# Kernel optimization log

Measured on AMD Instinct MI355X. Metric: run time of the kernel, lower is better.

## Reference

```python
import jax, jax.numpy as jnp
import numpy as np

N, E, F_IN = 100000, 3200000, 512
H1, D1, C = 8, 8, 16  # layer1 heads, per-head dim; layer2 out classes
NEG_SLOPE = 0.2


def _segment_softmax(e, dst, num_segments):
    # numerically-stable softmax over edges grouped by destination node
    m = jax.ops.segment_max(e, dst, num_segments=num_segments)
    ex = jnp.exp(e - m[dst])
    s = jax.ops.segment_sum(ex, dst, num_segments=num_segments)
    return ex / (s[dst] + 1e-16)


def _gat_layer(x, src, dst, W, a_src, a_dst, heads, d_out):
    n = x.shape[0]
    h = (x @ W).reshape(n, heads, d_out)          # [N,H,D]
    al_s = jnp.einsum('nhd,hd->nh', h, a_src)     # [N,H]
    al_d = jnp.einsum('nhd,hd->nh', h, a_dst)
    e = jax.nn.leaky_relu(al_s[src] + al_d[dst], NEG_SLOPE)  # [E,H]
    alpha = _segment_softmax(e, dst, n)           # [E,H]
    msg = h[src] * alpha[..., None]               # [E,H,D]
    return jax.ops.segment_sum(msg, dst, num_segments=n)  # [N,H,D]


def setup_inputs() -> dict:
    key = jax.random.key(0)
    ks = jax.random.split(key, 8)
    x = jax.random.normal(ks[0], (N, F_IN), dtype=jnp.float32)
    edge_index = jax.random.randint(ks[1], (2, E), 0, N, dtype=jnp.int64)
    W1 = jax.random.normal(ks[2], (F_IN, H1 * D1), dtype=jnp.float32) * (1.0 / np.sqrt(F_IN))
    a1_src = jax.random.normal(ks[3], (H1, D1), dtype=jnp.float32)
    a1_dst = jax.random.normal(ks[4], (H1, D1), dtype=jnp.float32)
    W2 = jax.random.normal(ks[5], (H1 * D1, C), dtype=jnp.float32) * (1.0 / np.sqrt(H1 * D1))
    a2_src = jax.random.normal(ks[6], (1, C), dtype=jnp.float32)
    a2_dst = jax.random.normal(ks[7], (1, C), dtype=jnp.float32)
    return {'x': x, 'edge_index': edge_index, 'W1': W1, 'a1_src': a1_src,
            'a1_dst': a1_dst, 'W2': W2, 'a2_src': a2_src, 'a2_dst': a2_dst}


def reference(x, edge_index, W1, a1_src, a1_dst, W2, a2_src, a2_dst):
    src, dst = edge_index[0], edge_index[1]
    # layer 1: 8 heads, concat, then ELU (dropout is identity in eval mode)
    h1 = _gat_layer(x, src, dst, W1, a1_src, a1_dst, H1, D1)  # [N,H1,D1]
    h1 = jax.nn.elu(h1.reshape(N, H1 * D1))                   # [N,64]
    # layer 2: single head -> class logits
    h2 = _gat_layer(h1, src, dst, W2, a2_src, a2_dst, 1, C)   # [N,1,C]
    return jax.nn.log_softmax(h2.reshape(N, C), axis=1)
```

## Files before the change

### kernel.cpp

```cpp
#include <hip/hip_runtime.h>
#include <math.h>

#define NEG 0.2f
#define NB 64
#define BCAP 128

typedef __attribute__((ext_vector_type(8))) short bf16x8;
typedef __attribute__((ext_vector_type(4))) float f32x4;
typedef unsigned long long ull;

static __device__ __forceinline__ float lrelu(float x){ return x > 0.f ? x : NEG*x; }

static __device__ __forceinline__ void bsplit(float v, unsigned int& hi, unsigned int& lo){
  unsigned int u = __float_as_uint(v);
  unsigned int hb = (u + 0x7fffu + ((u >> 16) & 1u)) & 0xffff0000u;
  float hf = __uint_as_float(hb);
  float l = v - hf;
  unsigned int ul = __float_as_uint(l);
  hi = hb >> 16;
  lo = (ul + 0x7fffu + ((ul >> 16) & 1u)) >> 16;
}

static __device__ __forceinline__ float bf2f(unsigned short u){
  return __uint_as_float(((unsigned int)u) << 16);
}
static __device__ __forceinline__ unsigned short f2bf(float v){
  unsigned int u = __float_as_uint(v);
  return (unsigned short)((u + 0x7fffu + ((u >> 16) & 1u)) >> 16);
}

static __device__ __forceinline__ void split8(float4 v0, float4 v1, bf16x8& h, bf16x8& l){
  float vv[8] = {v0.x, v0.y, v0.z, v0.w, v1.x, v1.y, v1.z, v1.w};
  #pragma unroll
  for (int i = 0; i < 8; ++i) {
    unsigned int hi, lo;
    bsplit(vv[i], hi, lo);
    h[i] = (short)hi;
    l[i] = (short)lo;
  }
}

__global__ void k_zero(int* __restrict__ p, int n){
  int i = blockIdx.x*blockDim.x + threadIdx.x;
  if (i < n) p[i] = 0;
}

__global__ void k_flag(const int* __restrict__ u, int* __restrict__ flag){
  if (threadIdx.x == 0 && blockIdx.x == 0) {
    int z = 1;
    for (int e = 0; e < 64; ++e) if (u[2*e+1] != 0) { z = 0; break; }
    *flag = z;
  }
}

__global__ __launch_bounds__(256) void k_part(const int* __restrict__ u,
    const int* __restrict__ flag, int* __restrict__ pcur,
    ull* __restrict__ part, int E, int n, int SEGCAP){
  __shared__ ull buf[NB][BCAP];
  __shared__ int bcnt[NB];
  __shared__ int binc[NB];
  __shared__ int bbase;
  __shared__ int nflush;
  __shared__ unsigned char flist[NB];
  const bool f = (*flag) != 0;
  const int tid = threadIdx.x;
  const int g = blockIdx.x & 7;
  if (tid < NB) bcnt[tid] = 0;
  const long long stride = (long long)gridDim.x * 256;
  const long long iters = ((long long)E + stride - 1) / stride;
  long long e = (long long)blockIdx.x*256 + tid;
  for (long long it = 0; it < iters; ++it, e += stride) {
    if (tid < NB) binc[tid] = 0;
    if (tid == 0) nflush = 0;
    __syncthreads();
    int src = 0, dst = 0, b = 0;
    const bool valid = (e < E);
    if (valid) {
      src = f ? u[2*e] : u[e];
      dst = f ? u[2*(E+e)] : u[E+e];
      b = (int)(((long long)dst * NB) / n);
      atomicAdd(&binc[b], 1);
    }
    __syncthreads();
    if (tid < NB && bcnt[tid] > 0 && bcnt[tid] + binc[tid] > BCAP) {
      int i = atomicAdd(&nflush, 1);
      flist[i] = (unsigned char)tid;
    }
    __syncthreads();
    for (int i = 0; i < nflush; ++i) {
      int b2 = flist[i];
      int c = bcnt[b2]; if (c > BCAP) c = BCAP;
      if (tid == 0) bbase = atomicAdd(&pcur[(b2*8+g)*16], c);
      __syncthreads();
      int base = bbase;
      for (int j = tid; j < c; j += 256) {
        int pos = base + j;
        if (pos < SEGCAP) part[(size_t)(b2*8+g)*SEGCAP + pos] = buf[b2][j];
      }
      __syncthreads();
      if (tid == 0) bcnt[b2] = 0;
      __syncthreads();
    }
    if (valid) {
      int pos = atomicAdd(&bcnt[b], 1);
      if (pos < BCAP) buf[b][pos] = (ull)(unsigned)src | ((ull)(unsigned)dst << 32);
    }
    __syncthreads();
  }
  for (int b2 = 0; b2 < NB; ++b2) {
    int c = bcnt[b2]; if (c > BCAP) c = BCAP;
    if (c > 0) {
      if (tid == 0) bbase = atomicAdd(&pcur[(b2*8+g)*16], c);
      __syncthreads();
      int base = bbase;
      for (int j = tid; j < c; j += 256) {
        int pos = base + j;
        if (pos < SEGCAP) part[(size_t)(b2*8+g)*SEGCAP + pos] = buf[b2][j];
      }
    }
    __syncthreads();
  }
}

__global__ __launch_bounds__(1024) void k_histL(const int* __restrict__ pcur,
    const ull* __restrict__ part, int* __restrict__ cnt, int n, int SEGCAP){
  __shared__ int lcnt[1664];
  const int b = blockIdx.x;
  const int lo = (int)(((long long)b * n + NB - 1) / NB);
  const int hi = (int)(((long long)(b+1) * n + NB - 1) / NB);
  const int m = hi - lo;
  for (int i = threadIdx.x; i < m; i += 1024) lcnt[i] = 0;
  __syncthreads();
  for (int g = 0; g < 8; ++g) {
    int s = b*8 + g;
    int c = pcur[s*16]; if (c > SEGCAP) c = SEGCAP;
    for (int i = threadIdx.x; i < c; i += 1024) {
      ull v = __builtin_nontemporal_load(&part[(size_t)s*SEGCAP + i]);
      atomicAdd(&lcnt[(int)(unsigned)(v >> 32) - lo], 1);
    }
  }
  __syncthreads();
  for (int i = threadIdx.x; i < m; i += 1024) cnt[lo + i] = lcnt[i];
}

__global__ __launch_bounds__(256) void k_scan1(const int* __restrict__ cnt,
    int* __restrict__ ro, int* __restrict__ bsum, int n){
  int t = threadIdx.x;
  int base = blockIdx.x*1024 + t*4;
  int v0 = (base+0 < n) ? cnt[base+0] : 0;
  int v1 = (base+1 < n) ? cnt[base+1] : 0;
  int v2 = (base+2 < n) ? cnt[base+2] : 0;
  int v3 = (base+3 < n) ? cnt[base+3] : 0;
  int s = v0+v1+v2+v3;
  int lane = t & 63, w = t >> 6;
  int inc = s;
  for (int off = 1; off < 64; off <<= 1) {
    int tm = __shfl_up(inc, off);
    if (lane >= off) inc += tm;
  }
  __shared__ int wsum[4];
  if (lane == 63) wsum[w] = inc;
  __syncthreads();
  int wpre = 0;
  for (int k = 0; k < 4; ++k) if (k < w) wpre += wsum[k];
  int run = wpre + inc - s;
  if (base+0 < n) ro[base+0] = run; run += v0;
  if (base+1 < n) ro[base+1] = run; run += v1;
  if (base+2 < n) ro[base+2] = run; run += v2;
  if (base+3 < n) ro[base+3] = run; run += v3;
  if (t == 255) bsum[blockIdx.x] = run;
}

__global__ void k_scan2(int* __restrict__ bsum, int nb){
  int lane = threadIdx.x;
  int carry = 0;
  for (int b = 0; b < nb; b += 64) {
    int i = b + lane;
    int v = (i < nb) ? bsum[i] : 0;
    int inc = v;
    for (int off = 1; off < 64; off <<= 1) {
      int t = __shfl_up(inc, off);
      if (lane >= off) inc += t;
    }
    if (i < nb) bsum[i] = carry + inc - v;
    carry += __shfl(inc, 63);
  }
}

__global__ void k_scan3(int* __restrict__ ro, const int* __restrict__ bsum,
                        int n, int E){
  int i = blockIdx.x*blockDim.x + threadIdx.x;
  if (i < n) ro[i] = ro[i] + bsum[i >> 10];
  if (i == 0) ro[n] = E;
}

__global__ __launch_bounds__(1024) void k_fillL(const int* __restrict__ pcur,
    const ull* __restrict__ part, const int* __restrict__ ro,
    int* __restrict__ csr, int n, int SEGCAP){
  __shared__ int lcur[1664];
  const int b = blockIdx.x;
  const int lo = (int)(((long long)b * n + NB - 1) / NB);
  const int hi = (int)(((long long)(b+1) * n + NB - 1) / NB);
  const int m = hi - lo;
  for (int i = threadIdx.x; i < m; i += 1024) lcur[i] = ro[lo + i];
  __syncthreads();
  for (int g = 0; g < 8; ++g) {
    int s = b*8 + g;
    int c = pcur[s*16]; if (c > SEGCAP) c = SEGCAP;
    for (int i = threadIdx.x; i < c; i += 1024) {
      ull v = __builtin_nontemporal_load(&part[(size_t)s*SEGCAP + i]);
      int src = (int)(unsigned)v;
      int dst = (int)(unsigned)(v >> 32);
      int p = atomicAdd(&lcur[dst - lo], 1);
      csr[p] = src;
    }
  }
}

__global__ void k_wprep(const float* __restrict__ W1, unsigned short* __restrict__ wtH,
                        unsigned short* __restrict__ wtL){
  int i = blockIdx.x*256 + threadIdx.x;
  if (i >= 512*64) return;
  int k = i >> 6, c = i & 63;
  unsigned int hi, lo;
  bsplit(W1[i], hi, lo);
  wtH[c*512 + k] = (unsigned short)hi;
  wtL[c*512 + k] = (unsigned short)lo;
}

__global__ __launch_bounds__(256, 3) void k_proj1(const float* __restrict__ x,
    const unsigned short* __restrict__ wtH, const unsigned short* __restrict__ wtL,
    const float* __restrict__ a1s_g, const float* __restrict__ a1d_g,
    unsigned short* __restrict__ h1bf, float* __restrict__ al1s, float* __restrict__ al1d, int n){
  const int tid = threadIdx.x;
  const int lane = tid & 63;
  const int w = tid >> 6;
  const int l16 = lane & 15;
  const int lhi = lane >> 4;
  const int r0 = blockIdx.x*128 + w*32;

  float as_c[4], ad_c[4];
  #pragma unroll
  for (int f = 0; f < 4; ++f) { as_c[f] = a1s_g[16*f + l16]; ad_c[f] = a1d_g[16*f + l16]; }

  f32x4 acc[2][4];
  #pragma unroll
  for (int m = 0; m < 2; ++m)
    #pragma unroll
    for (int f = 0; f < 4; ++f) acc[m][f] = (f32x4){0.f,0.f,0.f,0.f};

  int rowA = r0 + l16;        if (rowA >= n) rowA = n - 1;
  int rowB = r0 + 16 + l16;   if (rowB >= n) rowB = n - 1;
  const float* xA = x + (size_t)rowA*512 + 8*lhi;
  const float* xB = x + (size_t)rowB*512 + 8*lhi;
  const unsigned short* wHp = wtH + (size_t)l16*512 + 8*lhi;
  const unsigned short* wLp = wtL + (size_t)l16*512 + 8*lhi;

  for (int k0 = 0; k0 < 512; k0 += 32) {
    float4 a0 = *(const float4*)(xA + k0);
    float4 a1v = *(const float4*)(xA + k0 + 4);
    float4 b0 = *(const float4*)(xB + k0);
    float4 b1v = *(const float4*)(xB + k0 + 4);
    bf16x8 bh[4], bl[4];
    #pragma unroll
    for (int f = 0; f < 4; ++f) {
      bh[f] = *(const bf16x8*)(wHp + (size_t)f*16*512 + k0);
      bl[f] = *(const bf16x8*)(wLp + (size_t)f*16*512 + k0);
    }
    bf16x8 ahA, alA, ahB, alB;
    split8(a0, a1v, ahA, alA);
    split8(b0, b1v, ahB, alB);
    #pragma unroll
    for (int f = 0; f < 4; ++f) {
      acc[0][f] = __builtin_amdgcn_mfma_f32_16x16x32_bf16(ahA, bh[f], acc[0][f], 0, 0, 0);
      acc[0][f] = __builtin_amdgcn_mfma_f32_16x16x32_bf16(ahA, bl[f], acc[0][f], 0, 0, 0);
      acc[0][f] = __builtin_amdgcn_mfma_f32_16x16x32_bf16(alA, bh[f], acc[0][f], 0, 0, 0);
      acc[1][f] = __builtin_amdgcn_mfma_f32_16x16x32_bf16(ahB, bh[f], acc[1][f], 0, 0, 0);
      acc[1][f] = __builtin_amdgcn_mfma_f32_16x16x32_bf16(ahB, bl[f], acc[1][f], 0, 0, 0);
      acc[1][f] = __builtin_amdgcn_mfma_f32_16x16x32_bf16(alB, bh[f], acc[1][f], 0, 0, 0);
    }
  }

  #pragma unroll
  for (int m = 0; m < 2; ++m) {
    #pragma unroll
    for (int r = 0; r < 4; ++r) {
      int node = r0 + 16*m + 4*lhi + r;
      bool ok = (node < n);
      #pragma unroll
      for (int f = 0; f < 4; ++f) {
        float v = acc[m][f][r];
        if (ok) h1bf[(size_t)node*64 + 16*f + l16] = f2bf(v);
        float vs = v * as_c[f], vd = v * ad_c[f];
        vs += __shfl_xor(vs, 1); vs += __shfl_xor(vs, 2); vs += __shfl_xor(vs, 4);
        vd += __shfl_xor(vd, 1); vd += __shfl_xor(vd, 2); vd += __shfl_xor(vd, 4);
        if (ok && (l16 & 7) == 0) {
          int head = 2*f + (l16 >> 3);
          al1s[node*8 + head] = vs;
          al1d[node*8 + head] = vd;
        }
      }
    }
  }
}

__global__ __launch_bounds__(256) void k_agg1(const int* __restrict__ ro,
    const int* __restrict__ csr, const float* __restrict__ al1s,
    const float* __restrict__ al1d, const unsigned short* __restrict__ h1bf,
    float* __restrict__ h1b, int n){
  int wid = blockIdx.x*4 + (threadIdx.x >> 6);
  if (wid >= n) return;
  int node = __builtin_amdgcn_readfirstlane(wid);
  int lane = threadIdx.x & 63;
  int h = lane >> 3;
  int beg = ro[node], end = ro[node+1];
  float ald = al1d[node*8 + h];
  float s = 0.f, acc = 0.f;
  if (beg < end) {
    int   srcb[4];
    float alb[4], hvb[4];
    #pragma unroll
    for (int j = 0; j < 4; ++j) {
      int idx = beg + j;
      srcb[j] = csr[idx < end ? idx : beg];
    }
    #pragma unroll
    for (int j = 0; j < 4; ++j) {
      alb[j] = al1s[srcb[j]*8 + h];
      hvb[j] = bf2f(h1bf[(size_t)srcb[j]*64 + lane]);
    }
    for (int t = beg; t < end; t += 4) {
      int   nsrc[4];
      float nal[4], nhv[4];
      #pragma unroll
      for (int j = 0; j < 4; ++j) {
        int idx = t + 4 + j;
        nsrc[j] = csr[idx < end ? idx : beg];
      }
      #pragma unroll
      for (int j = 0; j < 4; ++j) {
        nal[j] = al1s[nsrc[j]*8 + h];
        nhv[j] = bf2f(h1bf[(size_t)nsrc[j]*64 + lane]);
      }
      #pragma unroll
      for (int j = 0; j < 4; ++j) {
        float e = alb[j] + ald;
        e = e > 0.f ? e : NEG*e;
        float ex = (t + j < end) ? __expf(e) : 0.f;
        s += ex;
        acc = fmaf(hvb[j], ex, acc);
      }
      #pragma unroll
      for (int j = 0; j < 4; ++j) { srcb[j] = nsrc[j]; alb[j] = nal[j]; hvb[j] = nhv[j]; }
    }
  }
  float v = acc / (s + 1e-16f);
  v = v > 0.f ? v : expm1f(v);
  h1b[(size_t)node*64 + lane] = v;
}

__global__ __launch_bounds__(256) void k_proj2(const float* __restrict__ h1b,
    const float* __restrict__ W2, const float* __restrict__ a2s_g, const float* __restrict__ a2d_g,
    unsigned short* __restrict__ h2bf, float* __restrict__ al2s, float* __restrict__ al2d, int n){
  __shared__ float w[64*16];
  __shared__ float a2sv[16], a2dv[16];
  for (int i = threadIdx.x; i < 1024; i += 256) w[i] = W2[i];
  if (threadIdx.x < 16) { a2sv[threadIdx.x] = a2s_g[threadIdx.x]; a2dv[threadIdx.x] = a2d_g[threadIdx.x]; }
  __syncthreads();
  int c = threadIdx.x & 15;
  int nid = blockIdx.x*16 + (threadIdx.x >> 4);
  if (nid >= n) return;
  const float* row = h1b + (size_t)nid*64;
  float acc = 0.f;
  #pragma unroll
  for (int k0 = 0; k0 < 64; k0 += 4) {
    float4 r = *(const float4*)(row + k0);
    acc = fmaf(r.x, w[(k0+0)*16 + c], acc);
    acc = fmaf(r.y, w[(k0+1)*16 + c], acc);
    acc = fmaf(r.z, w[(k0+2)*16 + c], acc);
    acc = fmaf(r.w, w[(k0+3)*16 + c], acc);
  }
  h2bf[(size_t)nid*16 + c] = f2bf(acc);
  float vs = acc * a2sv[c], vd = acc * a2dv[c];
  vs += __shfl_xor(vs, 1); vs += __shfl_xor(vs, 2); vs += __shfl_xor(vs, 4); vs += __shfl_xor(vs, 8);
  vd += __shfl_xor(vd, 1); vd += __shfl_xor(vd, 2); vd += __shfl_xor(vd, 4); vd += __shfl_xor(vd, 8);
  if (c == 0) { al2s[nid] = vs; al2d[nid] = vd; }
}

__global__ __launch_bounds__(256) void k_agg2(const int* __restrict__ ro,
    const int* __restrict__ csr, const float* __restrict__ al2s,
    const float* __restrict__ al2d, const unsigned short* __restrict__ h2bf,
    float* __restrict__ out, int n){
  int wid = blockIdx.x*4 + (threadIdx.x >> 6);
  if (wid >= n) return;
  int node = __builtin_amdgcn_readfirstlane(wid);
  int lane = threadIdx.x & 63;
  int j = lane >> 4, c = lane & 15;
  int beg = ro[node], end = ro[node+1];
  float ald = al2d[node];
  float sp = 0.f, acc = 0.f;
  if (beg < end) {
    int i = beg + j;
    int sA = csr[i < end ? i : beg];
    float aA = al2s[sA];
    float hA = bf2f(h2bf[(size_t)sA*16 + c]);
    for (; i < end; i += 4) {
      int i2 = i + 4;
      int sB = csr[i2 < end ? i2 : beg];
      float aB = al2s[sB];
      float hB = bf2f(h2bf[(size_t)sB*16 + c]);
      float e = lrelu(aA + ald);
      float ex = __expf(e);
      sp += ex;
      acc = fmaf(ex, hA, acc);
      sA = sB; aA = aB; hA = hB;
    }
  }
  sp  += __shfl_xor(sp, 16);  sp  += __shfl_xor(sp, 32);
  acc += __shfl_xor(acc, 16); acc += __shfl_xor(acc, 32);
  float v = acc / (sp + 1e-16f);
  float mx = v;
  mx = fmaxf(mx, __shfl_xor(mx, 1)); mx = fmaxf(mx, __shfl_xor(mx, 2));
  mx = fmaxf(mx, __shfl_xor(mx, 4)); mx = fmaxf(mx, __shfl_xor(mx, 8));
  float l = v - mx;
  float se = __expf(l);
  se += __shfl_xor(se, 1); se += __shfl_xor(se, 2);
  se += __shfl_xor(se, 4); se += __shfl_xor(se, 8);
  float res = l - logf(se);
  if (j == 0) out[(size_t)node*16 + c] = res;
}

static inline size_t alignup(size_t x){ return (x + 255) & ~(size_t)255; }

extern "C" void kernel_launch(void* const* d_in, const int* in_sizes, int n_in,
                              void* d_out, int out_size, void* d_ws, size_t ws_size,
                              hipStream_t stream){
  const float* x   = (const float*)d_in[0];
  const int*   ei  = (const int*)  d_in[1];
  const float* W1  = (const float*)d_in[2];
  const float* a1s = (const float*)d_in[3];
  const float* a1d = (const float*)d_in[4];
  const float* W2  = (const float*)d_in[5];
  const float* a2s = (const float*)d_in[6];
  const float* a2d = (const float*)d_in[7];
  float* out = (float*)d_out;

  const int n = in_sizes[0] / 512;
  const int E = in_sizes[1] / 2;

  char* w = (char*)d_ws;
  unsigned short* h1bf = (unsigned short*)w; w += alignup((size_t)n*64*2);
  float* h1b  = (float*)w; w += alignup((size_t)n*64*4);
  float* al1s_ = (float*)w; w += alignup((size_t)n*8*4);
  float* al1d_ = (float*)w; w += alignup((size_t)n*8*4);
  unsigned short* h2bf = (unsigned short*)w; w += alignup((size_t)n*16*2);
  float* al2s_ = (float*)w; w += alignup((size_t)n*4);
  float* al2d_ = (float*)w; w += alignup((size_t)n*4);
  int* cnt    = (int*)w;   w += alignup((size_t)n*4);
  int* ro     = (int*)w;   w += alignup((size_t)(n+1)*4);
  int* csr    = (int*)w;   w += alignup((size_t)E*4);
  int* bsum   = (int*)w;   w += alignup(512*4);
  int* flag   = (int*)w;   w += alignup(64);
  int* pcur   = (int*)w;   w += alignup((size_t)NB*8*16*4);
  unsigned short* wtH = (unsigned short*)w; w += alignup(512*64*2);
  unsigned short* wtL = (unsigned short*)w; w += alignup(512*64*2);

  ull* part = (ull*)h1bf;
  const int SEGCAP = 9300;

  const int nb_scan = (n + 1023) / 1024;

  k_zero<<<(NB*8*16 + 255)/256, 256, 0, stream>>>(pcur, NB*8*16);
  k_flag<<<1, 64, 0, stream>>>(ei, flag);
  k_wprep<<<128, 256, 0, stream>>>(W1, wtH, wtL);
  k_part<<<1024, 256, 0, stream>>>(ei, flag, pcur, part, E, n, SEGCAP);
  k_histL<<<NB, 1024, 0, stream>>>(pcur, part, cnt, n, SEGCAP);
  k_scan1<<<nb_scan, 256, 0, stream>>>(cnt, ro, bsum, n);
  k_scan2<<<1, 64, 0, stream>>>(bsum, nb_scan);
  k_scan3<<<(n+255)/256, 256, 0, stream>>>(ro, bsum, n, E);
  k_fillL<<<NB, 1024, 0, stream>>>(pcur, part, ro, csr, n, SEGCAP);

  k_proj1<<<(n+127)/128, 256, 0, stream>>>(x, wtH, wtL, a1s, a1d, h1bf, al1s_, al1d_, n);
  k_agg1<<<(n+3)/4, 256, 0, stream>>>(ro, csr, al1s_, al1d_, h1bf, h1b, n);
  k_proj2<<<(n+15)/16, 256, 0, stream>>>(h1b, W2, a2s, a2d, h2bf, al2s_, al2d_, n);
  k_agg2<<<(n+3)/4, 256, 0, stream>>>(ro, csr, al2s_, al2d_, h2bf, out, n);
}
```

Before: 515.7 us.

## Shrink proj1 tile to 16 rows per wave and software-prefetch next K slice

Result: slower. 550.7 us (+6.8%).

```diff
diff --git a/kernel.cpp b/kernel.cpp
--- a/kernel.cpp
+++ b/kernel.cpp
@@ -228,7 +228,7 @@
   wtL[c*512 + k] = (unsigned short)lo;
 }
 
-__global__ __launch_bounds__(256, 3) void k_proj1(const float* __restrict__ x,
+__global__ __launch_bounds__(256, 4) void k_proj1(const float* __restrict__ x,
     const unsigned short* __restrict__ wtH, const unsigned short* __restrict__ wtL,
     const float* __restrict__ a1s_g, const float* __restrict__ a1d_g,
     unsigned short* __restrict__ h1bf, float* __restrict__ al1s, float* __restrict__ al1d, int n){
@@ -237,68 +237,68 @@
   const int w = tid >> 6;
   const int l16 = lane & 15;
   const int lhi = lane >> 4;
-  const int r0 = blockIdx.x*128 + w*32;
+  const int r0 = blockIdx.x*64 + w*16;
 
   float as_c[4], ad_c[4];
   #pragma unroll
   for (int f = 0; f < 4; ++f) { as_c[f] = a1s_g[16*f + l16]; ad_c[f] = a1d_g[16*f + l16]; }
 
-  f32x4 acc[2][4];
-  #pragma unroll
-  for (int m = 0; m < 2; ++m)
-    #pragma unroll
-    for (int f = 0; f < 4; ++f) acc[m][f] = (f32x4){0.f,0.f,0.f,0.f};
-
-  int rowA = r0 + l16;        if (rowA >= n) rowA = n - 1;
-  int rowB = r0 + 16 + l16;   if (rowB >= n) rowB = n - 1;
-  const float* xA = x + (size_t)rowA*512 + 8*lhi;
-  const float* xB = x + (size_t)rowB*512 + 8*lhi;
+  f32x4 acc[4];
+  #pragma unroll
+  for (int f = 0; f < 4; ++f) acc[f] = (f32x4){0.f,0.f,0.f,0.f};
+
+  int row = r0 + l16; if (row >= n) row = n - 1;
+  const float* xp = x + (size_t)row*512 + 8*lhi;
   const unsigned short* wHp = wtH + (size_t)l16*512 + 8*lhi;
   const unsigned short* wLp = wtL + (size_t)l16*512 + 8*lhi;
 
+  float4 a0 = *(const float4*)(xp);
+  float4 a1v = *(const float4*)(xp + 4);
+  bf16x8 bh[4], bl[4];
+  #pragma unroll
+  for (int f = 0; f < 4; ++f) {
+    bh[f] = *(const bf16x8*)(wHp + f*8192);
+    bl[f] = *(const bf16x8*)(wLp + f*8192);
+  }
+
   for (int k0 = 0; k0 < 512; k0 += 32) {
-    float4 a0 = *(const float4*)(xA + k0);
-    float4 a1v = *(const float4*)(xA + k0 + 4);
-    float4 b0 = *(const float4*)(xB + k0);
-    float4 b1v = *(const float4*)(xB + k0 + 4);
-    bf16x8 bh[4], bl[4];
+    const int k1 = (k0 + 32 < 512) ? k0 + 32 : 0;
+    float4 na0 = *(const float4*)(xp + k1);
+    float4 na1 = *(const float4*)(xp + k1 + 4);
+    bf16x8 nbh[4], nbl[4];
     #pragma unroll
     for (int f = 0; f < 4; ++f) {
-      bh[f] = *(const bf16x8*)(wHp + (size_t)f*16*512 + k0);
-      bl[f] = *(const bf16x8*)(wLp + (size_t)f*16*512 + k0);
-    }
-    bf16x8 ahA, alA, ahB, alB;
-    split8(a0, a1v, ahA, alA);
-    split8(b0, b1v, ahB, alB);
+      nbh[f] = *(const bf16x8*)(wHp + f*8192 + k1);
+      nbl[f] = *(const bf16x8*)(wLp + f*8192 + k1);
+    }
+    bf16x8 ah, al_;
+    split8(a0, a1v, ah, al_);
     #pragma unroll
     for (int f = 0; f < 4; ++f) {
-      acc[0][f] = __builtin_amdgcn_mfma_f32_16x16x32_bf16(ahA, bh[f], acc[0][f], 0, 0, 0);
-      acc[0][f] = __builtin_amdgcn_mfma_f32_16x16x32_bf16(ahA, bl[f], acc[0][f], 0, 0, 0);
-      acc[0][f] = __builtin_amdgcn_mfma_f32_16x16x32_bf16(alA, bh[f], acc[0][f], 0, 0, 0);
-      acc[1][f] = __builtin_amdgcn_mfma_f32_16x16x32_bf16(ahB, bh[f], acc[1][f], 0, 0, 0);
-      acc[1][f] = __builtin_amdgcn_mfma_f32_16x16x32_bf16(ahB, bl[f], acc[1][f], 0, 0, 0);
-      acc[1][f] = __builtin_amdgcn_mfma_f32_16x16x32_bf16(alB, bh[f], acc[1][f], 0, 0, 0);
-    }
-  }
-
-  #pragma unroll
-  for (int m = 0; m < 2; ++m) {
-    #pragma unroll
-    for (int r = 0; r < 4; ++r) {
-      int node = r0 + 16*m + 4*lhi + r;
-      bool ok = (node < n);
-      #pragma unroll
-      for (int f = 0; f < 4; ++f) {
-        float v = acc[m][f][r];
-        if (ok) h1bf[(size_t)node*64 + 16*f + l16] = f2bf(v);
-        float vs = v * as_c[f], vd = v * ad_c[f];
-        vs += __shfl_xor(vs, 1); vs += __shfl_xor(vs, 2); vs += __shfl_xor(vs, 4);
-        vd += __shfl_xor(vd, 1); vd += __shfl_xor(vd, 2); vd += __shfl_xor(vd, 4);
-        if (ok && (l16 & 7) == 0) {
-          int head = 2*f + (l16 >> 3);
-          al1s[node*8 + head] = vs;
-          al1d[node*8 + head] = vd;
-        }
+      acc[f] = __builtin_amdgcn_mfma_f32_16x16x32_bf16(ah,  bh[f], acc[f], 0, 0, 0);
+      acc[f] = __builtin_amdgcn_mfma_f32_16x16x32_bf16(ah,  bl[f], acc[f], 0, 0, 0);
+      acc[f] = __builtin_amdgcn_mfma_f32_16x16x32_bf16(al_, bh[f], acc[f], 0, 0, 0);
+    }
+    a0 = na0; a1v = na1;
+    #pragma unroll
+    for (int f = 0; f < 4; ++f) { bh[f] = nbh[f]; bl[f] = nbl[f]; }
+  }
+
+  #pragma unroll
+  for (int r = 0; r < 4; ++r) {
+    int node = r0 + 4*lhi + r;
+    bool ok = (node < n);
+    #pragma unroll
+    for (int f = 0; f < 4; ++f) {
+      float v = acc[f][r];
+      if (ok) h1bf[(size_t)node*64 + 16*f + l16] = f2bf(v);
+      float vs = v * as_c[f], vd = v * ad_c[f];
+      vs += __shfl_xor(vs, 1); vs += __shfl_xor(vs, 2); vs += __shfl_xor(vs, 4);
+      vd += __shfl_xor(vd, 1); vd += __shfl_xor(vd, 2); vd += __shfl_xor(vd, 4);
+      if (ok && (l16 & 7) == 0) {
+        int head = 2*f + (l16 >> 3);
+        al1s[node*8 + head] = vs;
+        al1d[node*8 + head] = vd;
       }
     }
   }
@@ -480,7 +480,7 @@
   k_scan3<<<(n+255)/256, 256, 0, stream>>>(ro, bsum, n, E);
   k_fillL<<<NB, 1024, 0, stream>>>(pcur, part, ro, csr, n, SEGCAP);
 
-  k_proj1<<<(n+127)/128, 256, 0, stream>>>(x, wtH, wtL, a1s, a1d, h1bf, al1s_, al1d_, n);
+  k_proj1<<<(n+63)/64, 256, 0, stream>>>(x, wtH, wtL, a1s, a1d, h1bf, al1s_, al1d_, n);
   k_agg1<<<(n+3)/4, 256, 0, stream>>>(ro, csr, al1s_, al1d_, h1bf, h1b, n);
   k_proj2<<<(n+15)/16, 256, 0, stream>>>(h1b, W2, a2s, a2d, h2bf, al2s_, al2d_, n);
   k_agg2<<<(n+3)/4, 256, 0, stream>>>(ro, csr, al2s_, al2d_, h2bf, out, n);
```

## Stage x tiles through swizzled LDS with register prefetch in proj1

Applied to the files above, without the earlier changes.

New measurement: 561.5 us. +8.9%, slower.

```diff
diff --git a/kernel.cpp b/kernel.cpp
--- a/kernel.cpp
+++ b/kernel.cpp
@@ -228,16 +228,18 @@
   wtL[c*512 + k] = (unsigned short)lo;
 }
 
-__global__ __launch_bounds__(256, 3) void k_proj1(const float* __restrict__ x,
+__global__ __launch_bounds__(256) void k_proj1(const float* __restrict__ x,
     const unsigned short* __restrict__ wtH, const unsigned short* __restrict__ wtL,
     const float* __restrict__ a1s_g, const float* __restrict__ a1d_g,
     unsigned short* __restrict__ h1bf, float* __restrict__ al1s, float* __restrict__ al1d, int n){
+  __shared__ float xs[128*64];
   const int tid = threadIdx.x;
   const int lane = tid & 63;
   const int w = tid >> 6;
   const int l16 = lane & 15;
   const int lhi = lane >> 4;
-  const int r0 = blockIdx.x*128 + w*32;
+  const int n0 = blockIdx.x*128;
+  const int r0 = n0 + w*32;
 
   float as_c[4], ad_c[4];
   #pragma unroll
@@ -249,36 +251,61 @@
     #pragma unroll
     for (int f = 0; f < 4; ++f) acc[m][f] = (f32x4){0.f,0.f,0.f,0.f};
 
-  int rowA = r0 + l16;        if (rowA >= n) rowA = n - 1;
-  int rowB = r0 + 16 + l16;   if (rowB >= n) rowB = n - 1;
-  const float* xA = x + (size_t)rowA*512 + 8*lhi;
-  const float* xB = x + (size_t)rowB*512 + 8*lhi;
   const unsigned short* wHp = wtH + (size_t)l16*512 + 8*lhi;
   const unsigned short* wLp = wtL + (size_t)l16*512 + 8*lhi;
 
-  for (int k0 = 0; k0 < 512; k0 += 32) {
-    float4 a0 = *(const float4*)(xA + k0);
-    float4 a1v = *(const float4*)(xA + k0 + 4);
-    float4 b0 = *(const float4*)(xB + k0);
-    float4 b1v = *(const float4*)(xB + k0 + 4);
-    bf16x8 bh[4], bl[4];
+  const int srow = w*32 + (lane >> 4);
+  int g_row = n0 + srow;
+  const int chunk = (lane & 15);
+
+  float4 ld[8];
+  #pragma unroll
+  for (int i = 0; i < 8; ++i) {
+    int row = n0 + srow + i*4; if (row >= n) row = n - 1;
+    ld[i] = *(const float4*)(x + (size_t)row*512 + chunk*4);
+  }
+
+  for (int ks = 0; ks < 8; ++ks) {
+    const int k0 = ks*64;
     #pragma unroll
-    for (int f = 0; f < 4; ++f) {
-      bh[f] = *(const bf16x8*)(wHp + (size_t)f*16*512 + k0);
-      bl[f] = *(const bf16x8*)(wLp + (size_t)f*16*512 + k0);
-    }
-    bf16x8 ahA, alA, ahB, alB;
-    split8(a0, a1v, ahA, alA);
-    split8(b0, b1v, ahB, alB);
+    for (int i = 0; i < 8; ++i) {
+      int lr = srow + i*4;
+      int slot = chunk ^ (lr & 15);
+      *(float4*)&xs[lr*64 + slot*4] = ld[i];
+    }
+    __syncthreads();
+    if (ks < 7) {
+      #pragma unroll
+      for (int i = 0; i < 8; ++i) {
+        int row = n0 + srow + i*4; if (row >= n) row = n - 1;
+        ld[i] = *(const float4*)(x + (size_t)row*512 + (k0 + 64) + chunk*4);
+      }
+    }
     #pragma unroll
-    for (int f = 0; f < 4; ++f) {
-      acc[0][f] = __builtin_amdgcn_mfma_f32_16x16x32_bf16(ahA, bh[f], acc[0][f], 0, 0, 0);
-      acc[0][f] = __builtin_amdgcn_mfma_f32_16x16x32_bf16(ahA, bl[f], acc[0][f], 0, 0, 0);
-      acc[0][f] = __builtin_amdgcn_mfma_f32_16x16x32_bf16(alA, bh[f], acc[0][f], 0, 0, 0);
-      acc[1][f] = __builtin_amdgcn_mfma_f32_16x16x32_bf16(ahB, bh[f], acc[1][f], 0, 0, 0);
-      acc[1][f] = __builtin_amdgcn_mfma_f32_16x16x32_bf16(ahB, bl[f], acc[1][f], 0, 0, 0);
-      acc[1][f] = __builtin_amdgcn_mfma_f32_16x16x32_bf16(alB, bh[f], acc[1][f], 0, 0, 0);
-    }
+    for (int kk = 0; kk < 64; kk += 32) {
+      bf16x8 bh[4], bl[4];
+      #pragma unroll
+      for (int f = 0; f < 4; ++f) {
+        bh[f] = *(const bf16x8*)(wHp + (size_t)f*8192 + k0 + kk);
+        bl[f] = *(const bf16x8*)(wLp + (size_t)f*8192 + k0 + kk);
+      }
+      #pragma unroll
+      for (int m = 0; m < 2; ++m) {
+        int lr = w*32 + 16*m + l16;
+        int s0 = (kk >> 2) + 2*lhi;
+        float4 v0 = *(const float4*)&xs[lr*64 + ((s0 ^ (lr & 15)) << 2)];
+        float4 v1 = *(const float4*)&xs[lr*64 + (((s0 + 1) ^ (lr & 15)) << 2)];
+        bf16x8 ah, al_;
+        split8(v0, v1, ah, al_);
+        #pragma unroll
+        for (int f = 0; f < 4; ++f) {
+          acc[m][f] = __builtin_amdgcn_mfma_f32_16x16x32_bf16(ah,  bh[f], acc[m][f], 0, 0, 0);
+          acc[m][f] = __builtin_amdgcn_mfma_f32_16x16x32_bf16(ah,  bl[f], acc[m][f], 0, 0, 0);
+          acc[m][f] = __builtin_amdgcn_mfma_f32_16x16x32_bf16(al_, bh[f], acc[m][f], 0, 0, 0);
+        }
+      }
+    }
+    __syncthreads();
   }
 
   #pragma unroll
```
